# Optimization experiments

Hardware: AMD Instinct MI355X
Metric: run time of the kernel (lower is better)

## Reference

```python
import jax, jax.numpy as jnp
import numpy as np

N_CELLS = 196608  # 12 * 4**7 (HEALPix zoom 7)
NH = 9            # cell + 8 neighbors
F_IN = 64
F_OUT = 64


def setup_inputs() -> dict:
    key = jax.random.key(0)
    k1, k2, k3 = jax.random.split(key, 3)
    x = jax.random.normal(k1, (1, 1, 1, N_CELLS, F_IN), dtype=jnp.float32)
    adjc = jax.random.randint(k2, (N_CELLS, NH), 0, N_CELLS, dtype=jnp.int32)
    W = jax.random.normal(k3, (NH * F_IN, F_OUT), dtype=jnp.float32) * (1.0 / np.sqrt(NH * F_IN))
    return {"x": x, "adjc": adjc, "W": W}


def reference(x, adjc, W):
    # get_nh: gather neighborhood features along the cell axis.
    # x: [B, V, T, N, F], adjc: [N, NH] -> xnh: [B, V, T, N, NH, F]
    xnh = jnp.take(x, adjc, axis=3)
    B, V, T, N = xnh.shape[:4]
    # LinearLayer: flatten (NH, F) -> NH*F, dense projection to F_OUT (no bias)
    xf = xnh.reshape(B, V, T, N, NH * x.shape[-1])
    out = jnp.einsum('bvtnk,ko->bvtno', xf, W)  # [B, V, T, N, F_OUT]
    return out
```

## Files before the change

### kernel.cpp

```cpp
#include <hip/hip_runtime.h>
#include <hip/hip_bf16.h>
#include <stdint.h>

#define N_CELLS 196608
#define NH 9
#define F 64
#define K_TOT (NH * F)
#define K_STEPS (K_TOT / 32)
#define NFRAG (K_STEPS * 4)
#define WLDS_SHORTS (NFRAG * 64 * 8)
#define BLOCK 512

typedef __attribute__((ext_vector_type(8))) short bf16x8;
typedef __attribute__((ext_vector_type(4))) float f32x4;

__device__ inline unsigned short f2bf(float f) {
    union { float f; uint32_t u; } v; v.f = f;
    uint32_t u = v.u;
    uint32_t r = u + 0x7FFFu + ((u >> 16) & 1u);
    return (unsigned short)(r >> 16);
}

__global__ __launch_bounds__(256) void convert_x_kernel(
        const float* __restrict__ x, unsigned short* __restrict__ xb) {
    size_t i = (size_t)blockIdx.x * blockDim.x + threadIdx.x;
    const f32x4* p = reinterpret_cast<const f32x4*>(x);
    f32x4 a = p[i * 2], b = p[i * 2 + 1];
    unsigned short tmp[8];
    #pragma unroll
    for (int j = 0; j < 4; ++j) { tmp[j] = f2bf(a[j]); tmp[4 + j] = f2bf(b[j]); }
    *reinterpret_cast<bf16x8*>(xb + i * 8) = *reinterpret_cast<const bf16x8*>(tmp);
}

__global__ __launch_bounds__(256) void convert_w_kernel(
        const float* __restrict__ W, unsigned short* __restrict__ wb) {
    int tid = blockIdx.x * blockDim.x + threadIdx.x;
    int l = tid & 63;
    int frag = tid >> 6;
    int kk = frag >> 2, t = frag & 3;
    int k0 = kk * 32 + (l >> 4) * 8;
    int o  = t * 16 + (l & 15);
    unsigned short tmp[8];
    #pragma unroll
    for (int j = 0; j < 8; ++j) tmp[j] = f2bf(W[(size_t)(k0 + j) * F + o]);
    *reinterpret_cast<bf16x8*>(wb + (size_t)tid * 8) =
        *reinterpret_cast<const bf16x8*>(tmp);
}

template <bool XB>
__global__ __launch_bounds__(BLOCK, 2) void fused_gather_gemm_v8(
        const float* __restrict__ x32, const unsigned short* __restrict__ xb,
        const int* __restrict__ adjc, const unsigned short* __restrict__ wb,
        float* __restrict__ out) {
    __shared__ unsigned short wlds[WLDS_SHORTS];

    const int wave = threadIdx.x >> 6;
    const int lane = threadIdx.x & 63;
    const int lo = lane & 15, hi = lane >> 4;
    const int wcell = blockIdx.x * 256 + wave * 32;

    int idx[2][NH];
    #pragma unroll
    for (int m = 0; m < 2; ++m) {
        const int* ap = adjc + (size_t)(wcell + m * 16 + lo) * NH;
        #pragma unroll
        for (int j = 0; j < NH; ++j) idx[m][j] = __builtin_nontemporal_load(ap + j);
    }

    auto loadA = [&](int m, int j, int h) -> bf16x8 {
        if (XB) {
            return *reinterpret_cast<const bf16x8*>(
                    xb + (size_t)idx[m][j] * F + h * 32 + hi * 8);
        } else {
            const float* ap = x32 + (size_t)idx[m][j] * F + h * 32 + hi * 8;
            f32x4 f0 = *reinterpret_cast<const f32x4*>(ap);
            f32x4 f1 = *reinterpret_cast<const f32x4*>(ap + 4);
            unsigned short tmp[8];
            #pragma unroll
            for (int q = 0; q < 4; ++q) { tmp[q] = f2bf(f0[q]); tmp[4+q] = f2bf(f1[q]); }
            return *reinterpret_cast<const bf16x8*>(tmp);
        }
    };

    {
        const bf16x8* src = reinterpret_cast<const bf16x8*>(wb);
        bf16x8* dst = reinterpret_cast<bf16x8*>(wlds);
        #pragma unroll
        for (int it = 0; it < 9; ++it)
            dst[it * BLOCK + threadIdx.x] = src[it * BLOCK + threadIdx.x];
    }

    bf16x8 aS[3][2][2];
    #pragma unroll
    for (int m = 0; m < 2; ++m)
        #pragma unroll
        for (int h = 0; h < 2; ++h) {
            aS[0][m][h] = loadA(m, 0, h);
            aS[1][m][h] = loadA(m, 1, h);
        }
    __syncthreads();

    f32x4 acc[2][4];
    #pragma unroll
    for (int m = 0; m < 2; ++m)
        #pragma unroll
        for (int t = 0; t < 4; ++t) acc[m][t] = f32x4{0.f, 0.f, 0.f, 0.f};

    #pragma unroll
    for (int j = 0; j < NH; ++j) {
        const int cur = j % 3;
        const int nxt = (j + 2) % 3;
        if (j + 2 < NH) {
            #pragma unroll
            for (int m = 0; m < 2; ++m)
                #pragma unroll
                for (int h = 0; h < 2; ++h) aS[nxt][m][h] = loadA(m, j + 2, h);
        }
        __builtin_amdgcn_sched_barrier(0);
        #pragma unroll
        for (int h = 0; h < 2; ++h) {
            const int kk = j * 2 + h;
            #pragma unroll
            for (int t = 0; t < 4; ++t) {
                bf16x8 b = *reinterpret_cast<const bf16x8*>(
                        &wlds[((size_t)(kk * 4 + t) * 64 + lane) * 8]);
                #pragma unroll
                for (int m = 0; m < 2; ++m)
                    acc[m][t] = __builtin_amdgcn_mfma_f32_16x16x32_bf16(
                            aS[cur][m][h], b, acc[m][t], 0, 0, 0);
            }
        }
        __builtin_amdgcn_sched_barrier(0);
    }

    __syncthreads();
    float* ldsf = reinterpret_cast<float*>(wlds);
    const int rbase = wave * 2048;
    #pragma unroll
    for (int m = 0; m < 2; ++m)
        #pragma unroll
        for (int t = 0; t < 4; ++t)
            #pragma unroll
            for (int r = 0; r < 4; ++r)
                ldsf[rbase + (m * 16 + hi * 4 + r) * 64 + t * 16 + lo] =
                        acc[m][t][r];
    __syncthreads();
    #pragma unroll
    for (int p = 0; p < 8; ++p) {
        const int f = p * 256 + lane * 4;
        f32x4 v = *reinterpret_cast<const f32x4*>(&ldsf[rbase + f]);
        *reinterpret_cast<f32x4*>(&out[(size_t)wcell * F + f]) = v;
    }
}

__global__ void naive_kernel(const float* __restrict__ x,
                             const int* __restrict__ adjc,
                             const float* __restrict__ W,
                             float* __restrict__ out) {
    int n = blockIdx.x;
    int o = threadIdx.x;
    float acc = 0.f;
    for (int j = 0; j < NH; ++j) {
        int idx = adjc[(size_t)n * NH + j];
        for (int f = 0; f < F; ++f)
            acc += x[(size_t)idx * F + f] * W[(size_t)(j * F + f) * F + o];
    }
    out[(size_t)n * F + o] = acc;
}

extern "C" void kernel_launch(void* const* d_in, const int* in_sizes, int n_in,
                              void* d_out, int out_size, void* d_ws, size_t ws_size,
                              hipStream_t stream) {
    const float* x    = (const float*)d_in[0];
    const int*   adjc = (const int*)d_in[1];
    const float* W    = (const float*)d_in[2];
    float* out = (float*)d_out;

    const size_t need_x = (size_t)N_CELLS * F * sizeof(unsigned short);
    const size_t need_w = (size_t)K_TOT * F * sizeof(unsigned short);

    if (ws_size >= need_x + need_w) {
        unsigned short* xb = (unsigned short*)d_ws;
        unsigned short* wb = (unsigned short*)((char*)d_ws + need_x);
        convert_x_kernel<<<(N_CELLS * F / 8) / 256, 256, 0, stream>>>(x, xb);
        convert_w_kernel<<<(K_STEPS * 4 * 64) / 256, 256, 0, stream>>>(W, wb);
        fused_gather_gemm_v8<true><<<N_CELLS / 256, BLOCK, 0, stream>>>(
                x, xb, adjc, wb, out);
    } else if (ws_size >= need_w) {
        unsigned short* wb = (unsigned short*)d_ws;
        convert_w_kernel<<<(K_STEPS * 4 * 64) / 256, 256, 0, stream>>>(W, wb);
        fused_gather_gemm_v8<false><<<N_CELLS / 256, BLOCK, 0, stream>>>(
                x, nullptr, adjc, wb, out);
    } else {
        naive_kernel<<<N_CELLS, F, 0, stream>>>(x, adjc, W, out);
    }
}
```

Before: 62.44 us.

## Quantize gathered activations to int8 with per-row scales before fused gather-GEMM

```diff
diff --git a/kernel.cpp b/kernel.cpp
--- a/kernel.cpp
+++ b/kernel.cpp
@@ -21,15 +21,28 @@
     return (unsigned short)(r >> 16);
 }
 
-__global__ __launch_bounds__(256) void convert_x_kernel(
-        const float* __restrict__ x, unsigned short* __restrict__ xb) {
-    size_t i = (size_t)blockIdx.x * blockDim.x + threadIdx.x;
-    const f32x4* p = reinterpret_cast<const f32x4*>(x);
-    f32x4 a = p[i * 2], b = p[i * 2 + 1];
-    unsigned short tmp[8];
-    #pragma unroll
-    for (int j = 0; j < 4; ++j) { tmp[j] = f2bf(a[j]); tmp[4 + j] = f2bf(b[j]); }
-    *reinterpret_cast<bf16x8*>(xb + i * 8) = *reinterpret_cast<const bf16x8*>(tmp);
+__global__ __launch_bounds__(256) void convert_x_i8(
+        const float* __restrict__ x, signed char* __restrict__ xq,
+        float* __restrict__ stab) {
+    int gid = blockIdx.x * blockDim.x + threadIdx.x;
+    int row = gid >> 4;
+    int k   = (gid & 15) * 4;
+    f32x4 v = *reinterpret_cast<const f32x4*>(x + (size_t)row * F + k);
+    float m = fmaxf(fmaxf(fabsf(v[0]), fabsf(v[1])),
+                    fmaxf(fabsf(v[2]), fabsf(v[3])));
+    #pragma unroll
+    for (int d = 1; d < 16; d <<= 1) m = fmaxf(m, __shfl_xor(m, d, 64));
+    float s  = m * (1.0f / 127.0f);
+    float rs = (m > 0.f) ? 127.0f / m : 0.f;
+    int p = (((k & 31) >> 3) << 4) + ((k >> 5) << 3) + (k & 7);
+    unsigned int d = 0;
+    #pragma unroll
+    for (int q = 0; q < 4; ++q) {
+        int qi = (int)rintf(v[q] * rs);
+        d |= ((unsigned int)(qi & 0xff)) << (q * 8);
+    }
+    *reinterpret_cast<unsigned int*>(xq + (size_t)row * F + p) = d;
+    if ((gid & 15) == 0) stab[row] = s;
 }
 
 __global__ __launch_bounds__(256) void convert_w_kernel(
@@ -47,9 +60,8 @@
         *reinterpret_cast<const bf16x8*>(tmp);
 }
 
-template <bool XB>
-__global__ __launch_bounds__(BLOCK, 2) void fused_gather_gemm_v8(
-        const float* __restrict__ x32, const unsigned short* __restrict__ xb,
+__global__ __launch_bounds__(BLOCK, 2) void fused_gather_gemm_v9(
+        const signed char* __restrict__ xq, const float* __restrict__ stab,
         const int* __restrict__ adjc, const unsigned short* __restrict__ wb,
         float* __restrict__ out) {
     __shared__ unsigned short wlds[WLDS_SHORTS];
@@ -59,27 +71,30 @@
     const int lo = lane & 15, hi = lane >> 4;
     const int wcell = blockIdx.x * 256 + wave * 32;
 
-    int idx[2][NH];
+    int   idx[2][NH];
+    float sc[2][NH];
     #pragma unroll
     for (int m = 0; m < 2; ++m) {
         const int* ap = adjc + (size_t)(wcell + m * 16 + lo) * NH;
         #pragma unroll
         for (int j = 0; j < NH; ++j) idx[m][j] = __builtin_nontemporal_load(ap + j);
-    }
-
-    auto loadA = [&](int m, int j, int h) -> bf16x8 {
-        if (XB) {
-            return *reinterpret_cast<const bf16x8*>(
-                    xb + (size_t)idx[m][j] * F + h * 32 + hi * 8);
-        } else {
-            const float* ap = x32 + (size_t)idx[m][j] * F + h * 32 + hi * 8;
-            f32x4 f0 = *reinterpret_cast<const f32x4*>(ap);
-            f32x4 f1 = *reinterpret_cast<const f32x4*>(ap + 4);
-            unsigned short tmp[8];
-            #pragma unroll
-            for (int q = 0; q < 4; ++q) { tmp[q] = f2bf(f0[q]); tmp[4+q] = f2bf(f1[q]); }
-            return *reinterpret_cast<const bf16x8*>(tmp);
+        #pragma unroll
+        for (int j = 0; j < NH; ++j) sc[m][j] = stab[idx[m][j]];
+    }
+
+    auto loadA = [&](int m, int j) -> uint4 {
+        return *reinterpret_cast<const uint4*>(
+                xq + (size_t)idx[m][j] * F + hi * 16);
+    };
+    auto expand = [&](unsigned int d0, unsigned int d1, float s) -> bf16x8 {
+        unsigned short tmp[8];
+        #pragma unroll
+        for (int q = 0; q < 8; ++q) {
+            unsigned int dw = (q < 4) ? d0 : d1;
+            int c = (int)(signed char)((dw >> ((q & 3) * 8)) & 0xff);
+            tmp[q] = f2bf((float)c * s);
         }
+        return *reinterpret_cast<const bf16x8*>(tmp);
     };
 
     {
@@ -90,14 +105,12 @@
             dst[it * BLOCK + threadIdx.x] = src[it * BLOCK + threadIdx.x];
     }
 
-    bf16x8 aS[3][2][2];
-    #pragma unroll
-    for (int m = 0; m < 2; ++m)
-        #pragma unroll
-        for (int h = 0; h < 2; ++h) {
-            aS[0][m][h] = loadA(m, 0, h);
-            aS[1][m][h] = loadA(m, 1, h);
-        }
+    uint4 aS[3][2];
+    #pragma unroll
+    for (int m = 0; m < 2; ++m) {
+        aS[0][m] = loadA(m, 0);
+        aS[1][m] = loadA(m, 1);
+    }
     __syncthreads();
 
     f32x4 acc[2][4];
@@ -112,13 +125,18 @@
         const int nxt = (j + 2) % 3;
         if (j + 2 < NH) {
             #pragma unroll
-            for (int m = 0; m < 2; ++m)
-                #pragma unroll
-                for (int h = 0; h < 2; ++h) aS[nxt][m][h] = loadA(m, j + 2, h);
+            for (int m = 0; m < 2; ++m) aS[nxt][m] = loadA(m, j + 2);
         }
         __builtin_amdgcn_sched_barrier(0);
         #pragma unroll
         for (int h = 0; h < 2; ++h) {
+            bf16x8 a[2];
+            #pragma unroll
+            for (int m = 0; m < 2; ++m) {
+                unsigned int d0 = h ? aS[cur][m].z : aS[cur][m].x;
+                unsigned int d1 = h ? aS[cur][m].w : aS[cur][m].y;
+                a[m] = expand(d0, d1, sc[m][j]);
+            }
             const int kk = j * 2 + h;
             #pragma unroll
             for (int t = 0; t < 4; ++t) {
@@ -127,7 +145,7 @@
                 #pragma unroll
                 for (int m = 0; m < 2; ++m)
                     acc[m][t] = __builtin_amdgcn_mfma_f32_16x16x32_bf16(
-                            aS[cur][m][h], b, acc[m][t], 0, 0, 0);
+                            a[m], b, acc[m][t], 0, 0, 0);
             }
         }
         __builtin_amdgcn_sched_barrier(0);
@@ -176,21 +194,18 @@
     const float* W    = (const float*)d_in[2];
     float* out = (float*)d_out;
 
-    const size_t need_x = (size_t)N_CELLS * F * sizeof(unsigned short);
-    const size_t need_w = (size_t)K_TOT * F * sizeof(unsigned short);
-
-    if (ws_size >= need_x + need_w) {
-        unsigned short* xb = (unsigned short*)d_ws;
-        unsigned short* wb = (unsigned short*)((char*)d_ws + need_x);
-        convert_x_kernel<<<(N_CELLS * F / 8) / 256, 256, 0, stream>>>(x, xb);
+    const size_t need_xq = (size_t)N_CELLS * F;
+    const size_t need_s  = (size_t)N_CELLS * sizeof(float);
+    const size_t need_w  = (size_t)K_TOT * F * sizeof(unsigned short);
+
+    if (ws_size >= need_xq + need_s + need_w) {
+        signed char*    xq   = (signed char*)d_ws;
+        float*          stab = (float*)((char*)d_ws + need_xq);
+        unsigned short* wb   = (unsigned short*)((char*)d_ws + need_xq + need_s);
+        convert_x_i8<<<(N_CELLS * 16) / 256, 256, 0, stream>>>(x, xq, stab);
         convert_w_kernel<<<(K_STEPS * 4 * 64) / 256, 256, 0, stream>>>(W, wb);
-        fused_gather_gemm_v8<true><<<N_CELLS / 256, BLOCK, 0, stream>>>(
-                x, xb, adjc, wb, out);
-    } else if (ws_size >= need_w) {
-        unsigned short* wb = (unsigned short*)d_ws;
-        convert_w_kernel<<<(K_STEPS * 4 * 64) / 256, 256, 0, stream>>>(W, wb);
-        fused_gather_gemm_v8<false><<<N_CELLS / 256, BLOCK, 0, stream>>>(
-                x, nullptr, adjc, wb, out);
+        fused_gather_gemm_v9<<<N_CELLS / 256, BLOCK, 0, stream>>>(
+                xq, stab, adjc, wb, out);
     } else {
         naive_kernel<<<N_CELLS, F, 0, stream>>>(x, adjc, W, out);
     }
```

Measured after the change: 64.74 us. 1.04x slower.
